# Kernel optimization log

Hardware: AMD Instinct MI355X
Metric: run time of the kernel (lower is better)

## Reference

```python
import jax, jax.numpy as jnp
import numpy as np

B, CIN, L = 16, 256, 2048
HID, G, M = 512, 2, 512
LP = L // 2  # pooled length == hidden_length of patterns
BETA = 1.0


def setup_inputs() -> dict:
    key = jax.random.key(0)
    k = jax.random.split(key, 6)
    x = jax.random.normal(k[0], (B, CIN, L), dtype=jnp.float32)
    # ChannelPool: Conv1d(256 -> 512, kernel=1, groups=2): weight [512, 128, 1]
    w1 = jax.random.normal(k[1], (HID, CIN // G, 1), dtype=jnp.float32) * 0.05
    b1 = jax.random.normal(k[2], (HID,), dtype=jnp.float32) * 0.01
    # StatePattern memory bank: [num_memories, hidden_length]
    patterns = jax.random.normal(k[3], (M, LP), dtype=jnp.float32) * 0.02
    # Unpool: ConvTranspose1d(512 -> 256, kernel=2, stride=2, groups=2):
    # torch weight layout [in_channels, out_channels//groups, kernel] = [512, 128, 2]
    wT = jax.random.normal(k[4], (HID, CIN // G, 2), dtype=jnp.float32) * 0.05
    bT = jax.random.normal(k[5], (CIN,), dtype=jnp.float32) * 0.01
    RZ = jnp.array(0.1, dtype=jnp.float32)
    return {"x": x, "w1": w1, "b1": b1, "patterns": patterns, "wT": wT, "bT": bT, "RZ": RZ}


def reference(x, w1, b1, patterns, wT, bT, RZ):
    identity = x
    # --- grouped 1x1 conv (ChannelPool) ---
    # split channels into G groups: x [B,G,CIN/G,L], w [G,HID/G,CIN/G]
    xg = x.reshape(B, G, CIN // G, L)
    wg = w1[:, :, 0].reshape(G, HID // G, CIN // G)
    h = jnp.einsum('bgil,goi->bgol', xg, wg).reshape(B, HID, L) + b1[None, :, None]
    h = jax.nn.relu(h)  # act; norm1/dropout are identity (norm=False, eval)
    # --- MaxPool1d(kernel=2, stride=2) ---
    h = h.reshape(B, HID, LP, 2).max(axis=-1)  # [B, HID, LP]
    # --- Hopfield retrieval: softmax(beta * x @ P^T) @ P ---
    scores = jnp.einsum('bcl,ml->bcm', BETA * h, patterns)  # [B, HID, M]
    attn = jax.nn.softmax(scores, axis=-1)
    h = jnp.einsum('bcm,ml->bcl', attn, patterns)  # [B, HID, LP]
    # --- grouped ConvTranspose1d(k=2, s=2) ---
    hg = h.reshape(B, G, HID // G, LP)
    wtg = wT.reshape(G, HID // G, CIN // G, 2)
    y = jnp.einsum('bgil,giok->bgolk', hg, wtg)  # [B,G,CIN/G,LP,2]
    y = y.reshape(B, CIN, L) + bT[None, :, None]
    y = jax.nn.relu(y)  # act; norm2/dropout identity
    return identity + RZ * y
```

## Files before the change

kernel.cpp:

```cpp
#include <hip/hip_runtime.h>

#define NB 16
#define NCIN 256
#define NL 2048
#define NHID 512
#define NM 512
#define NLP 1024

typedef short bf16x8 __attribute__((ext_vector_type(8)));
typedef unsigned short u16x8 __attribute__((ext_vector_type(8)));
typedef float f32x4 __attribute__((ext_vector_type(4)));
typedef __attribute__((address_space(1))) const unsigned int gas_u32;
typedef __attribute__((address_space(3))) unsigned int las_u32;

__device__ __forceinline__ unsigned short f2bf(float f) {
    unsigned int u = __builtin_bit_cast(unsigned int, f);
    return (unsigned short)((u + 0x7FFFu + ((u >> 16) & 1u)) >> 16);
}
__device__ __forceinline__ float bf2f(unsigned short u) {
    return __builtin_bit_cast(float, ((unsigned int)u) << 16);
}

__global__ __launch_bounds__(512) void k_front(
    const float* __restrict__ x, const float* __restrict__ w1,
    const float* __restrict__ b1, const float* __restrict__ P,
    const float* __restrict__ wT, unsigned short* __restrict__ hb,
    unsigned short* __restrict__ Pb, unsigned short* __restrict__ Ptb,
    unsigned short* __restrict__ wTt)
{
    __shared__ __align__(16) unsigned short smem[66560];
    const int bb = blockIdx.x;
    const int t = threadIdx.x;

    if (bb >= 512) {
        if (bb < 640) {
            unsigned short (*tbuf)[65] = (unsigned short (*)[65])smem;
            const int pb = bb - 512;
            const int mt = pb >> 4, lt = pb & 15;
            for (int i = t; i < 4096; i += 512) {
                const int r = i >> 6, c = i & 63;
                const unsigned short v = f2bf(P[(size_t)(mt * 64 + r) * 1024 + lt * 64 + c]);
                Pb[(size_t)(mt * 64 + r) * 1024 + lt * 64 + c] = v;
                tbuf[c][r] = v;
            }
            __syncthreads();
            for (int i = t; i < 4096; i += 512) {
                const int r = i >> 6, c = i & 63;
                Ptb[(size_t)(lt * 64 + r) * 512 + mt * 64 + c] = tbuf[r][c];
            }
        } else {
            const int t5 = (bb - 640) * 512 + t;
            const int g = t5 >> 16, ok = (t5 >> 8) & 255, i = t5 & 255;
            wTt[t5] = f2bf(wT[(size_t)(g * 256 + i) * 256 + ok]);
        }
        return;
    }

    const int g  = bb & 1;
    const int rt = bb >> 1;
    const int r0 = rt * 128;
    const int b  = r0 >> 11, l0 = r0 & 2047;

    unsigned short* T   = smem;
    unsigned short* Asl = smem + 17408;
    unsigned short* Bsl = smem + 33792;
    unsigned short* epi = smem;

    #pragma unroll
    for (int i3 = 0; i3 < 8; ++i3) {
        const int idx = i3 * 512 + t;
        const int ch = idx >> 5, f4 = idx & 31;
        const float4 v = *(const float4*)(x + ((size_t)(b * 256 + g * 128 + ch)) * 2048 + l0 + f4 * 4);
        ushort4 u;
        u.x = f2bf(v.x); u.y = f2bf(v.y); u.z = f2bf(v.z); u.w = f2bf(v.w);
        *(ushort4*)(T + ch * 136 + f4 * 4) = u;
    }
    #pragma unroll
    for (int i5 = 0; i5 < 16; ++i5) {
        const int idx = i5 * 512 + t;
        const int o = idx >> 5, f4 = idx & 31;
        const float4 v = *(const float4*)(w1 + ((size_t)(g * 256 + o)) * 128 + f4 * 4);
        ushort4 u;
        u.x = f2bf(v.x); u.y = f2bf(v.y); u.z = f2bf(v.z); u.w = f2bf(v.w);
        *(ushort4*)(Bsl + o * 128 + f4 * 4) = u;
    }
    __syncthreads();
    #pragma unroll
    for (int i4 = 0; i4 < 4; ++i4) {
        const int idx = i4 * 512 + t;
        const int ch = idx & 127, lo = idx >> 7;
        const u16x8 v = *(const u16x8*)(T + ch * 136 + lo * 8);
        #pragma unroll
        for (int u2 = 0; u2 < 8; ++u2)
            Asl[(lo * 8 + u2) * 128 + ch] = v[u2];
    }
    __syncthreads();

    const int lane = t & 63, wave = t >> 6;
    const int wm = wave & 1, wn = wave >> 1;
    const int q = lane >> 4, lm = lane & 15;

    f32x4 acc[4][4];
    #pragma unroll
    for (int i = 0; i < 4; ++i)
        #pragma unroll
        for (int j = 0; j < 4; ++j)
            #pragma unroll
            for (int r = 0; r < 4; ++r) acc[i][j][r] = 0.f;

    #pragma unroll
    for (int kc = 0; kc < 4; ++kc) {
        bf16x8 af[4], bf[4];
        #pragma unroll
        for (int i = 0; i < 4; ++i)
            af[i] = *(const bf16x8*)(Asl + (wm * 64 + i * 16 + lm) * 128 + kc * 32 + q * 8);
        #pragma unroll
        for (int j = 0; j < 4; ++j)
            bf[j] = *(const bf16x8*)(Bsl + (wn * 64 + j * 16 + lm) * 128 + kc * 32 + q * 8);
        #pragma unroll
        for (int i = 0; i < 4; ++i)
            #pragma unroll
            for (int j = 0; j < 4; ++j)
                acc[i][j] = __builtin_amdgcn_mfma_f32_16x16x32_bf16(af[i], bf[j], acc[i][j], 0, 0, 0);
    }
    __syncthreads();

    #pragma unroll
    for (int j = 0; j < 4; ++j) {
        const int col = wn * 64 + j * 16 + lm;
        const float bias = b1[g * 256 + col];
        #pragma unroll
        for (int i = 0; i < 4; ++i) {
            const float p0 = fmaxf(fmaxf(acc[i][j][0], acc[i][j][1]) + bias, 0.f);
            const float p1 = fmaxf(fmaxf(acc[i][j][2], acc[i][j][3]) + bias, 0.f);
            const int lp_loc = wm * 32 + i * 8 + q * 2;
            ushort2 u; u.x = f2bf(p0); u.y = f2bf(p1);
            *(ushort2*)(epi + col * 72 + lp_loc) = u;
        }
    }
    __syncthreads();
    const int c_loc = t >> 1, half = t & 1;
    unsigned short* dst = hb + ((size_t)(b * 512 + g * 256 + c_loc)) * 1024 + (l0 >> 1) + half * 32;
    #pragma unroll
    for (int u = 0; u < 4; ++u)
        *(u16x8*)(dst + u * 8) = *(const u16x8*)(epi + c_loc * 72 + half * 32 + u * 8);
}

__global__ __launch_bounds__(256, 4) void gemm_sc(
    const unsigned short* __restrict__ A, const unsigned short* __restrict__ B,
    unsigned short* __restrict__ Sb)
{
    const int nt = blockIdx.x & 7;
    const int rt = blockIdx.x >> 3;
    const int r0 = rt * 128, n0 = nt * 64;

    __shared__ unsigned short Asl[128 * 64];
    __shared__ unsigned short Bsl[64 * 64];

    const int t = threadIdx.x;
    const int lane = t & 63;
    const int wave = t >> 6;
    const int wm = wave & 1, wn = wave >> 1;
    const int q = lane >> 4, lm = lane & 15;

    f32x4 acc[4][2];
    #pragma unroll
    for (int i = 0; i < 4; ++i)
        #pragma unroll
        for (int j = 0; j < 2; ++j)
            #pragma unroll
            for (int r = 0; r < 4; ++r) acc[i][j][r] = 0.f;

    for (int k0 = 0; k0 < 1024; k0 += 64) {
        #pragma unroll
        for (int rd = 0; rd < 4; ++rd) {
            const int e = rd * 2048 + t * 8;
            const int row = e >> 6, col = e & 63;
            const unsigned short* ga = A + (size_t)(r0 + row) * 1024 + k0 + col;
            __builtin_amdgcn_global_load_lds((gas_u32*)ga, (las_u32*)(Asl + e), 16, 0, 0);
        }
        #pragma unroll
        for (int rd = 0; rd < 2; ++rd) {
            const int e = rd * 2048 + t * 8;
            const int row = e >> 6, col = e & 63;
            const unsigned short* gb = B + (size_t)(n0 + row) * 1024 + k0 + col;
            __builtin_amdgcn_global_load_lds((gas_u32*)gb, (las_u32*)(Bsl + e), 16, 0, 0);
        }
        __syncthreads();
        #pragma unroll
        for (int kk = 0; kk < 2; ++kk) {
            bf16x8 af[4], bf[2];
            #pragma unroll
            for (int i = 0; i < 4; ++i)
                af[i] = *(const bf16x8*)(Asl + (wm * 64 + i * 16 + lm) * 64 + kk * 32 + q * 8);
            #pragma unroll
            for (int j = 0; j < 2; ++j)
                bf[j] = *(const bf16x8*)(Bsl + (wn * 32 + j * 16 + lm) * 64 + kk * 32 + q * 8);
            #pragma unroll
            for (int i = 0; i < 4; ++i)
                #pragma unroll
                for (int j = 0; j < 2; ++j)
                    acc[i][j] = __builtin_amdgcn_mfma_f32_16x16x32_bf16(af[i], bf[j], acc[i][j], 0, 0, 0);
        }
        __syncthreads();
    }

    #pragma unroll
    for (int i = 0; i < 4; ++i)
        #pragma unroll
        for (int j = 0; j < 2; ++j)
            #pragma unroll
            for (int r = 0; r < 4; ++r)
                Sb[(size_t)(r0 + wm * 64 + i * 16 + q * 4 + r) * 512
                   + n0 + wn * 32 + j * 16 + lm] = f2bf(acc[i][j][r]);
}

__global__ __launch_bounds__(256) void k_softmax(
    const unsigned short* __restrict__ Sb, unsigned short* __restrict__ Ab)
{
    const int row = blockIdx.x * 4 + (threadIdx.x >> 6);
    const int lane = threadIdx.x & 63;
    const u16x8 uv = *(const u16x8*)(Sb + (size_t)row * 512 + lane * 8);

    float v[8];
    #pragma unroll
    for (int j = 0; j < 8; ++j) v[j] = bf2f(uv[j]);

    float mx = v[0];
    #pragma unroll
    for (int j = 1; j < 8; ++j) mx = fmaxf(mx, v[j]);
    for (int off = 32; off > 0; off >>= 1) mx = fmaxf(mx, __shfl_xor(mx, off));

    float sum = 0.f;
    #pragma unroll
    for (int j = 0; j < 8; ++j) { v[j] = __expf(v[j] - mx); sum += v[j]; }
    for (int off = 32; off > 0; off >>= 1) sum += __shfl_xor(sum, off);

    const float inv = 1.f / sum;
    u16x8 ov;
    #pragma unroll
    for (int j = 0; j < 8; ++j) ov[j] = f2bf(v[j] * inv);
    *(u16x8*)(Ab + (size_t)row * 512 + lane * 8) = ov;
}

__global__ __launch_bounds__(256, 4) void gemm_retr(
    const unsigned short* __restrict__ Ptb, const unsigned short* __restrict__ Ab,
    unsigned short* __restrict__ h2T)
{
    const int tl = blockIdx.x & 63;
    const int b  = blockIdx.x >> 6;
    const int nt = tl & 7;
    const int rt = tl >> 3;
    const int r0 = rt * 128, n0 = nt * 64;

    __shared__ unsigned short Asl[128 * 64];
    __shared__ unsigned short Bsl[64 * 64];

    const int t = threadIdx.x;
    const int lane = t & 63;
    const int wave = t >> 6;
    const int wm = wave & 1, wn = wave >> 1;
    const int q = lane >> 4, lm = lane & 15;

    f32x4 acc[4][2];
    #pragma unroll
    for (int i = 0; i < 4; ++i)
        #pragma unroll
        for (int j = 0; j < 2; ++j)
            #pragma unroll
            for (int r = 0; r < 4; ++r) acc[i][j][r] = 0.f;

    for (int k0 = 0; k0 < 512; k0 += 64) {
        #pragma unroll
        for (int rd = 0; rd < 4; ++rd) {
            const int e = rd * 2048 + t * 8;
            const int row = e >> 6, col = e & 63;
            const unsigned short* ga = Ptb + (size_t)(r0 + row) * 512 + k0 + col;
            __builtin_amdgcn_global_load_lds((gas_u32*)ga, (las_u32*)(Asl + e), 16, 0, 0);
        }
        #pragma unroll
        for (int rd = 0; rd < 2; ++rd) {
            const int e = rd * 2048 + t * 8;
            const int row = e >> 6, col = e & 63;
            const unsigned short* gb = Ab + ((size_t)b * 512 + n0 + row) * 512 + k0 + col;
            __builtin_amdgcn_global_load_lds((gas_u32*)gb, (las_u32*)(Bsl + e), 16, 0, 0);
        }
        __syncthreads();
        #pragma unroll
        for (int kk = 0; kk < 2; ++kk) {
            bf16x8 af[4], bf[2];
            #pragma unroll
            for (int i = 0; i < 4; ++i)
                af[i] = *(const bf16x8*)(Asl + (wm * 64 + i * 16 + lm) * 64 + kk * 32 + q * 8);
            #pragma unroll
            for (int j = 0; j < 2; ++j)
                bf[j] = *(const bf16x8*)(Bsl + (wn * 32 + j * 16 + lm) * 64 + kk * 32 + q * 8);
            #pragma unroll
            for (int i = 0; i < 4; ++i)
                #pragma unroll
                for (int j = 0; j < 2; ++j)
                    acc[i][j] = __builtin_amdgcn_mfma_f32_16x16x32_bf16(af[i], bf[j], acc[i][j], 0, 0, 0);
        }
        __syncthreads();
    }

    #pragma unroll
    for (int i = 0; i < 4; ++i)
        #pragma unroll
        for (int j = 0; j < 2; ++j)
            #pragma unroll
            for (int r = 0; r < 4; ++r)
                h2T[((size_t)b * 1024 + r0 + wm * 64 + i * 16 + q * 4 + r) * 512
                    + n0 + wn * 32 + j * 16 + lm] = f2bf(acc[i][j][r]);
}

__global__ __launch_bounds__(256) void k4_gemm(
    const unsigned short* __restrict__ h2T, const unsigned short* __restrict__ wTt,
    const float* __restrict__ bT, const float* __restrict__ x,
    const float* __restrict__ RZ, float* __restrict__ out)
{
    const int nt = blockIdx.x & 1;
    const int g  = (blockIdx.x >> 1) & 1;
    const int rt = blockIdx.x >> 2;
    const int r0 = rt * 128;
    const int b  = r0 >> 10, lp0 = r0 & 1023;

    __shared__ __align__(16) char smem[65536];
    unsigned short* Asl = (unsigned short*)smem;
    unsigned short* Bsl = Asl + 128 * 64;
    float* epi = (float*)smem;

    const int t = threadIdx.x;
    const int lane = t & 63;
    const int wave = t >> 6;
    const int wm = wave & 1, wn = wave >> 1;
    const int q = lane >> 4, lm = lane & 15;

    f32x4 acc[4][4];
    #pragma unroll
    for (int i = 0; i < 4; ++i)
        #pragma unroll
        for (int j = 0; j < 4; ++j)
            #pragma unroll
            for (int r = 0; r < 4; ++r) acc[i][j][r] = 0.f;

    for (int k0 = 0; k0 < 256; k0 += 64) {
        #pragma unroll
        for (int rd = 0; rd < 4; ++rd) {
            const int e = rd * 2048 + t * 8;
            const int row = e >> 6, col = e & 63;
            const unsigned short* ga = h2T + (size_t)(r0 + row) * 512 + g * 256 + k0 + col;
            __builtin_amdgcn_global_load_lds((gas_u32*)ga, (las_u32*)(Asl + e), 16, 0, 0);
            const unsigned short* gb = wTt + (size_t)g * 65536 + (size_t)(nt * 128 + row) * 256 + k0 + col;
            __builtin_amdgcn_global_load_lds((gas_u32*)gb, (las_u32*)(Bsl + e), 16, 0, 0);
        }
        __syncthreads();
        #pragma unroll
        for (int kk = 0; kk < 2; ++kk) {
            bf16x8 af[4], bf[4];
            #pragma unroll
            for (int i = 0; i < 4; ++i)
                af[i] = *(const bf16x8*)(Asl + (wm * 64 + i * 16 + lm) * 64 + kk * 32 + q * 8);
            #pragma unroll
            for (int j = 0; j < 4; ++j)
                bf[j] = *(const bf16x8*)(Bsl + (wn * 64 + j * 16 + lm) * 64 + kk * 32 + q * 8);
            #pragma unroll
            for (int i = 0; i < 4; ++i)
                #pragma unroll
                for (int j = 0; j < 4; ++j)
                    acc[i][j] = __builtin_amdgcn_mfma_f32_16x16x32_bf16(af[i], bf[j], acc[i][j], 0, 0, 0);
        }
        __syncthreads();
    }

    #pragma unroll
    for (int j = 0; j < 4; ++j) {
        const int col_blk = wn * 64 + j * 16 + lm;
        const int o_l = col_blk >> 1, kk2 = col_blk & 1;
        #pragma unroll
        for (int i = 0; i < 4; ++i) {
            #pragma unroll
            for (int r = 0; r < 4; ++r) {
                const int row_l = wm * 64 + i * 16 + q * 4 + r;
                const int l_l = 2 * row_l + kk2;
                const int chunk = ((l_l >> 2) + o_l) & 63;
                epi[o_l * 256 + chunk * 4 + (l_l & 3)] = acc[i][j][r];
            }
        }
    }
    __syncthreads();
    const int row = t >> 2, quad = t & 3;
    const int c = g * 128 + nt * 64 + row;
    const float bias = bT[c];
    const float rz = RZ[0];
    const size_t gbase = ((size_t)(b * 256 + c)) * 2048 + 2 * lp0 + quad * 64;
    #pragma unroll
    for (int k = 0; k < 16; ++k) {
        const int chunk_phys = (quad * 16 + k + row) & 63;
        const float4 v = *(const float4*)(epi + row * 256 + chunk_phys * 4);
        const float4 xv = *(const float4*)(x + gbase + k * 4);
        float4 o;
        o.x = xv.x + rz * fmaxf(v.x + bias, 0.f);
        o.y = xv.y + rz * fmaxf(v.y + bias, 0.f);
        o.z = xv.z + rz * fmaxf(v.z + bias, 0.f);
        o.w = xv.w + rz * fmaxf(v.w + bias, 0.f);
        *(float4*)(out + gbase + k * 4) = o;
    }
}

extern "C" void kernel_launch(void* const* d_in, const int* in_sizes, int n_in,
                              void* d_out, int out_size, void* d_ws, size_t ws_size,
                              hipStream_t stream) {
    (void)in_sizes; (void)n_in; (void)out_size; (void)ws_size;
    const float* x  = (const float*)d_in[0];
    const float* w1 = (const float*)d_in[1];
    const float* b1 = (const float*)d_in[2];
    const float* P  = (const float*)d_in[3];
    const float* wT = (const float*)d_in[4];
    const float* bT = (const float*)d_in[5];
    const float* RZ = (const float*)d_in[6];
    float* out = (float*)d_out;

    char* ws = (char*)d_ws;
    unsigned short* hb  = (unsigned short*)ws;
    unsigned short* Ab  = (unsigned short*)ws;
    unsigned short* h2T = (unsigned short*)(ws + (16u << 20));
    unsigned short* Pb  = (unsigned short*)(ws + (32u << 20));
    unsigned short* Ptb = (unsigned short*)(ws + (33u << 20));
    unsigned short* wTt = (unsigned short*)(ws + (34u << 20));
    unsigned short* Sb  = (unsigned short*)out;

    hipLaunchKernelGGL(k_front,   dim3(896),  dim3(512), 0, stream,
                       x, w1, b1, P, wT, hb, Pb, Ptb, wTt);
    hipLaunchKernelGGL(gemm_sc,   dim3(512),  dim3(256), 0, stream, hb, Pb, Sb);
    hipLaunchKernelGGL(k_softmax, dim3(2048), dim3(256), 0, stream, Sb, Ab);
    hipLaunchKernelGGL(gemm_retr, dim3(1024), dim3(256), 0, stream, Ptb, Ab, h2T);
    hipLaunchKernelGGL(k4_gemm,   dim3(512),  dim3(256), 0, stream, h2T, wTt, bT, x, RZ, out);
}
```

Before: 182.8 us.

## Move Hopfield score and retrieval GEMMs to FP8 scaled MFMA

Stores the pooled activations, the pattern bank (pre-scaled by 64), its transpose and the softmax output (pre-scaled by 16) as FP8 instead of bf16. Both attention GEMMs then use the MI355X scaled 16x16x128 f8f6f4 MFMA, with block scale exponents undoing the pre-scaling. This halves operand bytes and doubles the K per instruction, cutting memory traffic and MFMA issue count. The cost is much lower precision in the scores and retrieval, which could break numerical tolerance.

```diff
diff --git a/kernel.cpp b/kernel.cpp
--- a/kernel.cpp
+++ b/kernel.cpp
@@ -10,8 +10,13 @@
 typedef short bf16x8 __attribute__((ext_vector_type(8)));
 typedef unsigned short u16x8 __attribute__((ext_vector_type(8)));
 typedef float f32x4 __attribute__((ext_vector_type(4)));
+typedef int i32x8 __attribute__((ext_vector_type(8)));
 typedef __attribute__((address_space(1))) const unsigned int gas_u32;
 typedef __attribute__((address_space(3))) unsigned int las_u32;
+
+#define SC_UNIT 0x7F7F7F7F
+#define SC_M6   0x79797979
+#define SC_M4   0x7B7B7B7B
 
 __device__ __forceinline__ unsigned short f2bf(float f) {
     unsigned int u = __builtin_bit_cast(unsigned int, f);
@@ -20,12 +25,23 @@
 __device__ __forceinline__ float bf2f(unsigned short u) {
     return __builtin_bit_cast(float, ((unsigned int)u) << 16);
 }
+__device__ __forceinline__ unsigned short f2fp8x2(float a, float b) {
+    return (unsigned short)(__builtin_amdgcn_cvt_pk_fp8_f32(a, b, 0, false) & 0xFFFF);
+}
+__device__ __forceinline__ unsigned char f2fp8(float a) {
+    return (unsigned char)(__builtin_amdgcn_cvt_pk_fp8_f32(a, 0.f, 0, false) & 0xFF);
+}
+__device__ __forceinline__ int f2fp8x4(float a, float b, float c, float d) {
+    int w = __builtin_amdgcn_cvt_pk_fp8_f32(a, b, 0, false);
+    w = __builtin_amdgcn_cvt_pk_fp8_f32(c, d, w, true);
+    return w;
+}
 
 __global__ __launch_bounds__(512) void k_front(
     const float* __restrict__ x, const float* __restrict__ w1,
     const float* __restrict__ b1, const float* __restrict__ P,
-    const float* __restrict__ wT, unsigned short* __restrict__ hb,
-    unsigned short* __restrict__ Pb, unsigned short* __restrict__ Ptb,
+    const float* __restrict__ wT, unsigned char* __restrict__ hb8,
+    unsigned char* __restrict__ Pb8, unsigned char* __restrict__ Ptb8,
     unsigned short* __restrict__ wTt)
 {
     __shared__ __align__(16) unsigned short smem[66560];
@@ -34,19 +50,19 @@
 
     if (bb >= 512) {
         if (bb < 640) {
-            unsigned short (*tbuf)[65] = (unsigned short (*)[65])smem;
+            unsigned char (*tbuf)[65] = (unsigned char (*)[65])smem;
             const int pb = bb - 512;
             const int mt = pb >> 4, lt = pb & 15;
             for (int i = t; i < 4096; i += 512) {
                 const int r = i >> 6, c = i & 63;
-                const unsigned short v = f2bf(P[(size_t)(mt * 64 + r) * 1024 + lt * 64 + c]);
-                Pb[(size_t)(mt * 64 + r) * 1024 + lt * 64 + c] = v;
+                const unsigned char v = f2fp8(P[(size_t)(mt * 64 + r) * 1024 + lt * 64 + c] * 64.f);
+                Pb8[(size_t)(mt * 64 + r) * 1024 + lt * 64 + c] = v;
                 tbuf[c][r] = v;
             }
             __syncthreads();
             for (int i = t; i < 4096; i += 512) {
                 const int r = i >> 6, c = i & 63;
-                Ptb[(size_t)(lt * 64 + r) * 512 + mt * 64 + c] = tbuf[r][c];
+                Ptb8[(size_t)(lt * 64 + r) * 512 + mt * 64 + c] = tbuf[r][c];
             }
         } else {
             const int t5 = (bb - 640) * 512 + t;
@@ -64,7 +80,7 @@
     unsigned short* T   = smem;
     unsigned short* Asl = smem + 17408;
     unsigned short* Bsl = smem + 33792;
-    unsigned short* epi = smem;
+    unsigned char*  epi = (unsigned char*)smem;
 
     #pragma unroll
     for (int i3 = 0; i3 < 8; ++i3) {
@@ -134,28 +150,26 @@
             const float p0 = fmaxf(fmaxf(acc[i][j][0], acc[i][j][1]) + bias, 0.f);
             const float p1 = fmaxf(fmaxf(acc[i][j][2], acc[i][j][3]) + bias, 0.f);
             const int lp_loc = wm * 32 + i * 8 + q * 2;
-            ushort2 u; u.x = f2bf(p0); u.y = f2bf(p1);
-            *(ushort2*)(epi + col * 72 + lp_loc) = u;
+            *(unsigned short*)(epi + col * 80 + lp_loc) = f2fp8x2(p0, p1);
         }
     }
     __syncthreads();
     const int c_loc = t >> 1, half = t & 1;
-    unsigned short* dst = hb + ((size_t)(b * 512 + g * 256 + c_loc)) * 1024 + (l0 >> 1) + half * 32;
-    #pragma unroll
-    for (int u = 0; u < 4; ++u)
-        *(u16x8*)(dst + u * 8) = *(const u16x8*)(epi + c_loc * 72 + half * 32 + u * 8);
-}
-
-__global__ __launch_bounds__(256, 4) void gemm_sc(
-    const unsigned short* __restrict__ A, const unsigned short* __restrict__ B,
+    unsigned char* dst = hb8 + ((size_t)(b * 512 + g * 256 + c_loc)) * 1024 + (l0 >> 1) + half * 32;
+    *(int4*)dst        = *(const int4*)(epi + c_loc * 80 + half * 32);
+    *(int4*)(dst + 16) = *(const int4*)(epi + c_loc * 80 + half * 32 + 16);
+}
+
+__global__ __launch_bounds__(256, 4) void gemm_sc8(
+    const unsigned char* __restrict__ A, const unsigned char* __restrict__ B,
     unsigned short* __restrict__ Sb)
 {
     const int nt = blockIdx.x & 7;
     const int rt = blockIdx.x >> 3;
     const int r0 = rt * 128, n0 = nt * 64;
 
-    __shared__ unsigned short Asl[128 * 64];
-    __shared__ unsigned short Bsl[64 * 64];
+    __shared__ unsigned char Asl[128 * 128];
+    __shared__ unsigned char Bsl[64 * 128];
 
     const int t = threadIdx.x;
     const int lane = t & 63;
@@ -171,37 +185,35 @@
             #pragma unroll
             for (int r = 0; r < 4; ++r) acc[i][j][r] = 0.f;
 
-    for (int k0 = 0; k0 < 1024; k0 += 64) {
+    for (int k0 = 0; k0 < 1024; k0 += 128) {
         #pragma unroll
         for (int rd = 0; rd < 4; ++rd) {
-            const int e = rd * 2048 + t * 8;
-            const int row = e >> 6, col = e & 63;
-            const unsigned short* ga = A + (size_t)(r0 + row) * 1024 + k0 + col;
+            const int e = rd * 4096 + t * 16;
+            const int row = e >> 7, col = e & 127;
+            const unsigned char* ga = A + (size_t)(r0 + row) * 1024 + k0 + col;
             __builtin_amdgcn_global_load_lds((gas_u32*)ga, (las_u32*)(Asl + e), 16, 0, 0);
         }
         #pragma unroll
         for (int rd = 0; rd < 2; ++rd) {
-            const int e = rd * 2048 + t * 8;
-            const int row = e >> 6, col = e & 63;
-            const unsigned short* gb = B + (size_t)(n0 + row) * 1024 + k0 + col;
+            const int e = rd * 4096 + t * 16;
+            const int row = e >> 7, col = e & 127;
+            const unsigned char* gb = B + (size_t)(n0 + row) * 1024 + k0 + col;
             __builtin_amdgcn_global_load_lds((gas_u32*)gb, (las_u32*)(Bsl + e), 16, 0, 0);
         }
         __syncthreads();
-        #pragma unroll
-        for (int kk = 0; kk < 2; ++kk) {
-            bf16x8 af[4], bf[2];
-            #pragma unroll
-            for (int i = 0; i < 4; ++i)
-                af[i] = *(const bf16x8*)(Asl + (wm * 64 + i * 16 + lm) * 64 + kk * 32 + q * 8);
+        i32x8 af[4], bf[2];
+        #pragma unroll
+        for (int i = 0; i < 4; ++i)
+            af[i] = *(const i32x8*)(Asl + (wm * 64 + i * 16 + lm) * 128 + q * 32);
+        #pragma unroll
+        for (int j = 0; j < 2; ++j)
+            bf[j] = *(const i32x8*)(Bsl + (wn * 32 + j * 16 + lm) * 128 + q * 32);
+        #pragma unroll
+        for (int i = 0; i < 4; ++i)
             #pragma unroll
             for (int j = 0; j < 2; ++j)
-                bf[j] = *(const bf16x8*)(Bsl + (wn * 32 + j * 16 + lm) * 64 + kk * 32 + q * 8);
-            #pragma unroll
-            for (int i = 0; i < 4; ++i)
-                #pragma unroll
-                for (int j = 0; j < 2; ++j)
-                    acc[i][j] = __builtin_amdgcn_mfma_f32_16x16x32_bf16(af[i], bf[j], acc[i][j], 0, 0, 0);
-        }
+                acc[i][j] = __builtin_amdgcn_mfma_scale_f32_16x16x128_f8f6f4(
+                    af[i], bf[j], acc[i][j], 0, 0, 0, SC_UNIT, 0, SC_M6);
         __syncthreads();
     }
 
@@ -216,7 +228,7 @@
 }
 
 __global__ __launch_bounds__(256) void k_softmax(
-    const unsigned short* __restrict__ Sb, unsigned short* __restrict__ Ab)
+    const unsigned short* __restrict__ Sb, unsigned char* __restrict__ Ab8)
 {
     const int row = blockIdx.x * 4 + (threadIdx.x >> 6);
     const int lane = threadIdx.x & 63;
@@ -236,15 +248,15 @@
     for (int j = 0; j < 8; ++j) { v[j] = __expf(v[j] - mx); sum += v[j]; }
     for (int off = 32; off > 0; off >>= 1) sum += __shfl_xor(sum, off);
 
-    const float inv = 1.f / sum;
-    u16x8 ov;
-    #pragma unroll
-    for (int j = 0; j < 8; ++j) ov[j] = f2bf(v[j] * inv);
-    *(u16x8*)(Ab + (size_t)row * 512 + lane * 8) = ov;
-}
-
-__global__ __launch_bounds__(256, 4) void gemm_retr(
-    const unsigned short* __restrict__ Ptb, const unsigned short* __restrict__ Ab,
+    const float inv16 = 16.f / sum;
+    int2 ov;
+    ov.x = f2fp8x4(v[0] * inv16, v[1] * inv16, v[2] * inv16, v[3] * inv16);
+    ov.y = f2fp8x4(v[4] * inv16, v[5] * inv16, v[6] * inv16, v[7] * inv16);
+    *(int2*)(Ab8 + (size_t)row * 512 + lane * 8) = ov;
+}
+
+__global__ __launch_bounds__(256, 4) void gemm_retr8(
+    const unsigned char* __restrict__ Ptb8, const unsigned char* __restrict__ Ab8,
     unsigned short* __restrict__ h2T)
 {
     const int tl = blockIdx.x & 63;
@@ -253,8 +265,8 @@
     const int rt = tl >> 3;
     const int r0 = rt * 128, n0 = nt * 64;
 
-    __shared__ unsigned short Asl[128 * 64];
-    __shared__ unsigned short Bsl[64 * 64];
+    __shared__ unsigned char Asl[128 * 128];
+    __shared__ unsigned char Bsl[64 * 128];
 
     const int t = threadIdx.x;
     const int lane = t & 63;
@@ -270,37 +282,35 @@
             #pragma unroll
             for (int r = 0; r < 4; ++r) acc[i][j][r] = 0.f;
 
-    for (int k0 = 0; k0 < 512; k0 += 64) {
+    for (int k0 = 0; k0 < 512; k0 += 128) {
         #pragma unroll
         for (int rd = 0; rd < 4; ++rd) {
-            const int e = rd * 2048 + t * 8;
-            const int row = e >> 6, col = e & 63;
-            const unsigned short* ga = Ptb + (size_t)(r0 + row) * 512 + k0 + col;
+            const int e = rd * 4096 + t * 16;
+            const int row = e >> 7, col = e & 127;
+            const unsigned char* ga = Ptb8 + (size_t)(r0 + row) * 512 + k0 + col;
             __builtin_amdgcn_global_load_lds((gas_u32*)ga, (las_u32*)(Asl + e), 16, 0, 0);
         }
         #pragma unroll
         for (int rd = 0; rd < 2; ++rd) {
-            const int e = rd * 2048 + t * 8;
-            const int row = e >> 6, col = e & 63;
-            const unsigned short* gb = Ab + ((size_t)b * 512 + n0 + row) * 512 + k0 + col;
+            const int e = rd * 4096 + t * 16;
+            const int row = e >> 7, col = e & 127;
+            const unsigned char* gb = Ab8 + ((size_t)b * 512 + n0 + row) * 512 + k0 + col;
             __builtin_amdgcn_global_load_lds((gas_u32*)gb, (las_u32*)(Bsl + e), 16, 0, 0);
         }
         __syncthreads();
-        #pragma unroll
-        for (int kk = 0; kk < 2; ++kk) {
-            bf16x8 af[4], bf[2];
-            #pragma unroll
-            for (int i = 0; i < 4; ++i)
-                af[i] = *(const bf16x8*)(Asl + (wm * 64 + i * 16 + lm) * 64 + kk * 32 + q * 8);
+        i32x8 af[4], bf[2];
+        #pragma unroll
+        for (int i = 0; i < 4; ++i)
+            af[i] = *(const i32x8*)(Asl + (wm * 64 + i * 16 + lm) * 128 + q * 32);
+        #pragma unroll
+        for (int j = 0; j < 2; ++j)
+            bf[j] = *(const i32x8*)(Bsl + (wn * 32 + j * 16 + lm) * 128 + q * 32);
+        #pragma unroll
+        for (int i = 0; i < 4; ++i)
             #pragma unroll
             for (int j = 0; j < 2; ++j)
-                bf[j] = *(const bf16x8*)(Bsl + (wn * 32 + j * 16 + lm) * 64 + kk * 32 + q * 8);
-            #pragma unroll
-            for (int i = 0; i < 4; ++i)
-                #pragma unroll
-                for (int j = 0; j < 2; ++j)
-                    acc[i][j] = __builtin_amdgcn_mfma_f32_16x16x32_bf16(af[i], bf[j], acc[i][j], 0, 0, 0);
-        }
+                acc[i][j] = __builtin_amdgcn_mfma_scale_f32_16x16x128_f8f6f4(
+                    af[i], bf[j], acc[i][j], 0, 0, 0, SC_M6, 0, SC_M4);
         __syncthreads();
     }
 
@@ -422,18 +432,18 @@
     float* out = (float*)d_out;
 
     char* ws = (char*)d_ws;
-    unsigned short* hb  = (unsigned short*)ws;
-    unsigned short* Ab  = (unsigned short*)ws;
-    unsigned short* h2T = (unsigned short*)(ws + (16u << 20));
-    unsigned short* Pb  = (unsigned short*)(ws + (32u << 20));
-    unsigned short* Ptb = (unsigned short*)(ws + (33u << 20));
-    unsigned short* wTt = (unsigned short*)(ws + (34u << 20));
-    unsigned short* Sb  = (unsigned short*)out;
-
-    hipLaunchKernelGGL(k_front,   dim3(896),  dim3(512), 0, stream,
-                       x, w1, b1, P, wT, hb, Pb, Ptb, wTt);
-    hipLaunchKernelGGL(gemm_sc,   dim3(512),  dim3(256), 0, stream, hb, Pb, Sb);
-    hipLaunchKernelGGL(k_softmax, dim3(2048), dim3(256), 0, stream, Sb, Ab);
-    hipLaunchKernelGGL(gemm_retr, dim3(1024), dim3(256), 0, stream, Ptb, Ab, h2T);
-    hipLaunchKernelGGL(k4_gemm,   dim3(512),  dim3(256), 0, stream, h2T, wTt, bT, x, RZ, out);
-}
+    unsigned char*  hb8  = (unsigned char*)ws;
+    unsigned char*  Ab8  = (unsigned char*)(ws + (8u << 20));
+    unsigned short* h2T  = (unsigned short*)(ws + (16u << 20));
+    unsigned char*  Pb8  = (unsigned char*)(ws + (32u << 20));
+    unsigned char*  Ptb8 = (unsigned char*)(ws + (32u << 20) + (512u << 10));
+    unsigned short* wTt  = (unsigned short*)(ws + (33u << 20));
+    unsigned short* Sb   = (unsigned short*)out;
+
+    hipLaunchKernelGGL(k_front,    dim3(896),  dim3(512), 0, stream,
+                       x, w1, b1, P, wT, hb8, Pb8, Ptb8, wTt);
+    hipLaunchKernelGGL(gemm_sc8,   dim3(512),  dim3(256), 0, stream, hb8, Pb8, Sb);
+    hipLaunchKernelGGL(k_softmax,  dim3(2048), dim3(256), 0, stream, Sb, Ab8);
+    hipLaunchKernelGGL(gemm_retr8, dim3(1024), dim3(256), 0, stream, Ptb8, Ab8, h2T);
+    hipLaunchKernelGGL(k4_gemm,    dim3(512),  dim3(256), 0, stream, h2T, wTt, bT, x, RZ, out);
+}
```

Measured after the change: 161.5 us. 11.6% less time.
